# Performance work log

Measured on AMD Instinct MI355X. Metric: run time of the kernel, lower is better.

The kernel has to match this reference:

```python
import jax, jax.numpy as jnp
import numpy as np

FRACTION = 0.33  # from attn_type='query_selector_0.33'


def setup_inputs() -> dict:
    key = jax.random.key(0)
    k1, k2, k3, k4 = jax.random.split(key, 4)
    B, L, DIM_VAL, DIM_ATTN = 8, 4096, 64, 64
    scale = 1.0 / np.sqrt(DIM_VAL).astype(np.float32)
    x = jax.random.normal(k1, (B, L, DIM_VAL), dtype=jnp.float32)
    Wq = jax.random.normal(k2, (DIM_VAL, DIM_ATTN), dtype=jnp.float32) * scale
    Wk = jax.random.normal(k3, (DIM_VAL, DIM_ATTN), dtype=jnp.float32) * scale
    Wv = jax.random.normal(k4, (DIM_VAL, DIM_VAL), dtype=jnp.float32) * scale
    return {"x": x, "Wq": Wq, "Wk": Wk, "Wv": Wv}


def reference(x, Wq, Wk, Wv):
    # Projections (bias-free Linears)
    Q = jnp.einsum('bld,de->ble', x, Wq)  # [B, L, Da]
    K = jnp.einsum('bld,de->ble', x, Wk)  # [B, L, Da]
    V = jnp.einsum('bld,de->ble', x, Wv)  # [B, L, Dv]

    B, L_Q, Da = Q.shape
    l_Q = int((1.0 - FRACTION) * L_Q)  # static: shapes known at trace time

    # keys.topk(l_Q, dim=1).values -> per-channel top-l_Q along seq; mean over them
    K_top = jax.lax.top_k(jnp.swapaxes(K, 1, 2), l_Q)[0]  # [B, Da, l_Q]
    K_reduce = K_top.mean(axis=-1)                         # [B, Da]

    # score each query against the reduced key; pick top-l_Q queries
    sqk = jnp.einsum('bd,bld->bl', K_reduce, Q)            # [B, L_Q]
    indices = jax.lax.top_k(sqk, l_Q)[1]                   # [B, l_Q] int32

    # gather sampled queries
    Q_sample = jnp.take_along_axis(Q, indices[:, :, None], axis=1)  # [B, l_Q, Da]

    # dense attention for the sampled queries only
    scores = jnp.einsum('bqd,bkd->bqk', Q_sample, K) / jnp.sqrt(jnp.asarray(Da, Q.dtype))
    attn = jax.nn.softmax(scores, axis=-1)                 # [B, l_Q, L]
    out_sel = jnp.einsum('bqk,bkv->bqv', attn, V)          # [B, l_Q, Dv]

    # mean-filled result, scatter attention outputs to selected rows
    mean_values = V.mean(axis=-2)                          # [B, Dv]
    result = jnp.broadcast_to(mean_values[:, None, :], (B, L_Q, V.shape[-1]))
    result = result.at[jnp.arange(B)[:, None], indices].set(out_sel)
    return result
```

## Files before the change

### kernel.cpp

```cpp
#include <hip/hip_runtime.h>
#include <hip/hip_bf16.h>
#include <math.h>

#define BATCH 8
#define SEQ   4096
#define DIM   64
#define LQ    2744
#define QPB   128
#define NQB   22
#define QPAD  2816
#define KS    4
#define L2E   1.4426950408889634f
#define QSC   0.1803368801111204f

typedef _Float16 half8 __attribute__((ext_vector_type(8)));
typedef short    bs8   __attribute__((ext_vector_type(8)));
typedef float    fx16  __attribute__((ext_vector_type(16)));
typedef unsigned short ushort_t;

union UH { uint4 u4; half8 h; };
union UB { unsigned u[4]; uint4 u4; bs8 s; };

__device__ __forceinline__ unsigned pack_bf16(float a, float b) {
    __hip_bfloat162 h = __float22bfloat162_rn(make_float2(a, b));
    union { __hip_bfloat162 h; unsigned u; } cv; cv.h = h; return cv.u;
}

__device__ __forceinline__ unsigned f2sort(float f) {
    unsigned u = __float_as_uint(f);
    return (u & 0x80000000u) ? ~u : (u | 0x80000000u);
}
__device__ __forceinline__ float sort2f(unsigned u) {
    return __uint_as_float((u & 0x80000000u) ? (u & 0x7FFFFFFFu) : ~u);
}

__device__ void radix_select_4096(const unsigned* u, int k, unsigned* hist,
                                  unsigned* scan, unsigned* res) {
    const int t = threadIdx.x;
    if (t == 0) { res[0] = 0u; res[1] = (unsigned)k; }
    for (int pass = 3; pass >= 0; --pass) {
        const int shift = pass * 8;
        hist[t] = 0u;
        __syncthreads();
        const unsigned pref  = res[0];
        const unsigned kk    = res[1];
        const unsigned hmask = (pass == 3) ? 0u : (0xFFFFFFFFu << (shift + 8));
        for (int i = t; i < 4096; i += 256) {
            unsigned ui = u[i];
            if ((ui & hmask) == pref) atomicAdd(&hist[(ui >> shift) & 255u], 1u);
        }
        __syncthreads();
        const unsigned h = hist[t];
        unsigned s = h;
        scan[t] = s;
        __syncthreads();
#pragma unroll
        for (int ofs = 1; ofs < 256; ofs <<= 1) {
            unsigned add = (t + ofs < 256) ? scan[t + ofs] : 0u;
            __syncthreads();
            s += add;
            scan[t] = s;
            __syncthreads();
        }
        if (s >= kk && (s - h) < kk) {
            res[0] = pref | ((unsigned)t << shift);
            res[1] = kk - (s - h);
        }
        __syncthreads();
    }
}

__global__ __launch_bounds__(256) void proj_kernel(
    const float* __restrict__ x,  const float* __restrict__ Wq,
    const float* __restrict__ Wk, const float* __restrict__ Wv,
    float* __restrict__ Q, float* __restrict__ Kt,
    _Float16* __restrict__ Qh, _Float16* __restrict__ Kh,
    ushort_t* __restrict__ Vt, float* __restrict__ pmean) {
    const int rt = blockIdx.x, b = blockIdx.y, t = threadIdx.x;
    __shared__ float4 xs4[64 * 17];
    __shared__ float  red[4][64];
    {
        const float4* xg = (const float4*)(x + ((size_t)b * SEQ + rt * 64) * DIM);
        for (int i = 0; i < 4; ++i) {
            int s = t + 256 * i;
            xs4[(s >> 4) * 17 + (s & 15)] = xg[s];
        }
    }
    __syncthreads();
    const int ch = t & 63, rg = t >> 6;
    float accq[16], acck[16], accv[16];
#pragma unroll
    for (int i = 0; i < 16; ++i) { accq[i] = 0.f; acck[i] = 0.f; accv[i] = 0.f; }
    for (int dc = 0; dc < 4; ++dc) {
        float wq[16], wk[16], wv[16];
#pragma unroll
        for (int dd = 0; dd < 16; ++dd) {
            int d = dc * 16 + dd;
            wq[dd] = Wq[d * 64 + ch]; wk[dd] = Wk[d * 64 + ch]; wv[dd] = Wv[d * 64 + ch];
        }
        for (int r = 0; r < 16; ++r) {
            const int row = rg * 16 + r;
            const float4* xr = &xs4[row * 17 + dc * 4];
            float xv[16];
            float4 a0 = xr[0], a1 = xr[1], a2 = xr[2], a3 = xr[3];
            xv[0]=a0.x; xv[1]=a0.y; xv[2]=a0.z; xv[3]=a0.w;
            xv[4]=a1.x; xv[5]=a1.y; xv[6]=a1.z; xv[7]=a1.w;
            xv[8]=a2.x; xv[9]=a2.y; xv[10]=a2.z; xv[11]=a2.w;
            xv[12]=a3.x; xv[13]=a3.y; xv[14]=a3.z; xv[15]=a3.w;
#pragma unroll
            for (int dd = 0; dd < 16; ++dd) {
                accq[r] = fmaf(xv[dd], wq[dd], accq[r]);
                acck[r] = fmaf(xv[dd], wk[dd], acck[r]);
                accv[r] = fmaf(xv[dd], wv[dd], accv[r]);
            }
        }
    }
    const int rowbase = rt * 64 + rg * 16;
    float sv = 0.f;
#pragma unroll
    for (int r = 0; r < 16; ++r) {
        size_t o = ((size_t)b * SEQ + rowbase + r) * DIM + ch;
        Q[o]  = accq[r];
        Qh[o] = (_Float16)(accq[r] * QSC);
        Kh[o] = (_Float16)acck[r];
        sv += accv[r];
    }
    float4* ktp = (float4*)(Kt + ((size_t)b * 64 + ch) * SEQ + rowbase);
    ktp[0] = make_float4(acck[0], acck[1], acck[2], acck[3]);
    ktp[1] = make_float4(acck[4], acck[5], acck[6], acck[7]);
    ktp[2] = make_float4(acck[8], acck[9], acck[10], acck[11]);
    ktp[3] = make_float4(acck[12], acck[13], acck[14], acck[15]);
    {
        unsigned pk[8];
#pragma unroll
        for (int i = 0; i < 8; ++i) pk[i] = pack_bf16(accv[2*i], accv[2*i+1]);
        uint4* vp = (uint4*)(Vt + ((size_t)(b * 64 + ch)) * SEQ + rowbase);
        vp[0] = make_uint4(pk[0], pk[1], pk[4], pk[5]);
        vp[1] = make_uint4(pk[2], pk[3], pk[6], pk[7]);
    }
    red[rg][ch] = sv;
    __syncthreads();
    if (rg == 0)
        pmean[((size_t)b * 64 + ch) * 64 + rt] =
            red[0][ch] + red[1][ch] + red[2][ch] + red[3][ch];
}

__global__ __launch_bounds__(256) void kmean_kernel(const float* __restrict__ Kt,
                                                    const float* __restrict__ pmean,
                                                    float* __restrict__ Kred,
                                                    float* __restrict__ meanfin) {
    __shared__ unsigned u[4096];
    __shared__ unsigned hist[256];
    __shared__ unsigned scan[256];
    __shared__ unsigned res[2];
    __shared__ float rsum[4];
    const int bc = blockIdx.x, t = threadIdx.x;
    if (t < 64) {
        float v = pmean[(size_t)bc * 64 + t];
        for (int m = 1; m < 64; m <<= 1) v += __shfl_xor(v, m, 64);
        if (t == 0) meanfin[bc] = v * (1.0f / (float)SEQ);
    }
    const float4* c4 = (const float4*)(Kt + (size_t)bc * SEQ);
    for (int i = t; i < 1024; i += 256) {
        float4 v = c4[i];
        u[i*4+0] = f2sort(v.x); u[i*4+1] = f2sort(v.y);
        u[i*4+2] = f2sort(v.z); u[i*4+3] = f2sort(v.w);
    }
    __syncthreads();
    radix_select_4096(u, LQ, hist, scan, res);
    const unsigned Tu = res[0];
    const int krem = (int)res[1];
    float loc = 0.f;
    for (int i = t; i < 4096; i += 256)
        if (u[i] > Tu) loc += sort2f(u[i]);
    for (int msk = 1; msk < 64; msk <<= 1) loc += __shfl_xor(loc, msk, 64);
    if ((t & 63) == 0) rsum[t >> 6] = loc;
    __syncthreads();
    if (t == 0) {
        float s = rsum[0] + rsum[1] + rsum[2] + rsum[3] + (float)krem * sort2f(Tu);
        Kred[bc] = s / (float)LQ;
    }
}

__global__ __launch_bounds__(256) void sqk_kernel(const float* __restrict__ Q,
                                                  const float* __restrict__ Kred,
                                                  float* __restrict__ sqk) {
    const int b = blockIdx.y, l = blockIdx.x * 256 + threadIdx.x;
    __shared__ float kr[64];
    if (threadIdx.x < 64) kr[threadIdx.x] = Kred[b * 64 + threadIdx.x];
    __syncthreads();
    const float4* q = (const float4*)(Q + ((size_t)b * SEQ + l) * DIM);
    float s = 0.f;
#pragma unroll
    for (int i = 0; i < 16; ++i) {
        float4 v = q[i];
        s = fmaf(v.x, kr[i*4+0], s); s = fmaf(v.y, kr[i*4+1], s);
        s = fmaf(v.z, kr[i*4+2], s); s = fmaf(v.w, kr[i*4+3], s);
    }
    sqk[b * SEQ + l] = s;
}

__global__ __launch_bounds__(256) void select_kernel(const float* __restrict__ sqk,
                                                     int* __restrict__ sel,
                                                     int* __restrict__ inv) {
    __shared__ unsigned u[4096];
    __shared__ unsigned hist[256];
    __shared__ unsigned scan[256];
    __shared__ unsigned res[2];
    __shared__ int eq_idx[256];
    __shared__ int cnts[2];
    const int b = blockIdx.x, t = threadIdx.x;
    const float* col = sqk + (size_t)b * SEQ;
    int* invb = inv + (size_t)b * SEQ;
    for (int i = t; i < 4096; i += 256) {
        u[i] = f2sort(col[i]);
        invb[i] = -1;
    }
    if (t < 2) cnts[t] = 0;
    __syncthreads();
    radix_select_4096(u, LQ, hist, scan, res);
    const unsigned Tu = res[0];
    const int krem = (int)res[1];
    int* selb = sel + b * QPAD;
    for (int i = t; i < 4096; i += 256) {
        unsigned ui = u[i];
        if (ui > Tu) {
            int p = atomicAdd(&cnts[0], 1);
            selb[p] = i;
            invb[i] = p;
        } else if (ui == Tu) {
            int p = atomicAdd(&cnts[1], 1);
            if (p < 256) eq_idx[p] = i;
        }
    }
    __syncthreads();
    if (t == 0) {
        int ng = cnts[0];
        int ne = cnts[1] < 256 ? cnts[1] : 256;
        for (int i = 1; i < ne; ++i) {
            int v = eq_idx[i], j = i - 1;
            while (j >= 0 && eq_idx[j] > v) { eq_idx[j+1] = eq_idx[j]; --j; }
            eq_idx[j+1] = v;
        }
        for (int j = 0; j < krem; ++j) {
            selb[ng + j] = eq_idx[j];
            invb[eq_idx[j]] = ng + j;
        }
    }
    __syncthreads();
    if (t < QPAD - LQ) selb[LQ + t] = selb[LQ - 1];
}

__global__ __launch_bounds__(256, 3) void attn_kernel(
    const ushort_t* __restrict__ Qh, const ushort_t* __restrict__ Kh,
    const ushort_t* __restrict__ Vt, const int* __restrict__ sel,
    float* __restrict__ pl, float* __restrict__ pout) {
    const int qt = blockIdx.x, ks = blockIdx.y, b = blockIdx.z;
    const int t = threadIdx.x, w = t >> 6, lane = t & 63;
    const int col = lane & 31, h = lane >> 5;

    __shared__ ushort_t Ktile[2][32 * 64];
    __shared__ ushort_t Vtile[2][32 * 64];

    half8 qf[4];
    {
        const int q = qt * QPB + w * 32 + col;
        const int row = sel[b * QPAD + q];
        const uint4* qg = (const uint4*)(Qh + ((size_t)b * SEQ + row) * DIM);
#pragma unroll
        for (int m = 0; m < 4; ++m) { UH u; u.u4 = qg[2 * m + h]; qf[m] = u.h; }
    }

    int koff[4], voff[4];
#pragma unroll
    for (int m = 0; m < 4; ++m)
        koff[m] = col * 64 + 8 * ((2 * m + h) ^ (col & 7));
#pragma unroll
    for (int i = 0; i < 4; ++i)
        voff[i] = col * 64 + 8 * ((i * 2 + h) ^ (col & 7));

    fx16 O0, O1;
#pragma unroll
    for (int r = 0; r < 16; ++r) { O0[r] = 0.f; O1[r] = 0.f; }
    float l = 0.f;

    const int srow = t >> 3, sgr = t & 7;
    const int lg = sgr ^ (srow & 7);
    const int vD = lg >> 2, vc = (lg >> 1) & 1, vh = lg & 1;
    const size_t kgbase = ((size_t)b * SEQ + ks * 1024 + srow) * DIM + 8 * lg;
    const size_t vgbase = ((size_t)(b * DIM + srow + 32 * vD)) * SEQ
                          + ks * 1024 + vc * 16 + vh * 8;

    uint4 kreg = *(const uint4*)(Kh + kgbase);
    uint4 vreg = *(const uint4*)(Vt + vgbase);

    for (int tile = 0; tile < 32; ++tile) {
        const int buf = tile & 1;
        *(uint4*)&Ktile[buf][srow * 64 + sgr * 8] = kreg;
        *(uint4*)&Vtile[buf][srow * 64 + sgr * 8] = vreg;
        __syncthreads();
        if (tile < 31) {
            kreg = *(const uint4*)(Kh + kgbase + (size_t)(tile + 1) * 32 * DIM);
            vreg = *(const uint4*)(Vt + vgbase + (size_t)(tile + 1) * 32);
        }
        fx16 S;
#pragma unroll
        for (int r = 0; r < 16; ++r) S[r] = 0.f;
#pragma unroll
        for (int m = 0; m < 4; ++m) {
            UH kf;
            kf.u4 = *(const uint4*)&Ktile[buf][koff[m]];
            S = __builtin_amdgcn_mfma_f32_32x32x16_f16(kf.h, qf[m], S, 0, 0, 0);
        }
        float p[16];
#pragma unroll
        for (int r = 0; r < 16; ++r) p[r] = exp2f(S[r]);
#pragma unroll
        for (int r = 0; r < 16; ++r) l += p[r];
        UB A0, A1;
#pragma unroll
        for (int v = 0; v < 4; ++v) {
            A0.u[v] = pack_bf16(p[2 * v],     p[2 * v + 1]);
            A1.u[v] = pack_bf16(p[8 + 2 * v], p[8 + 2 * v + 1]);
        }
#pragma unroll
        for (int D = 0; D < 2; ++D) {
            fx16& O = D ? O1 : O0;
#pragma unroll
            for (int c = 0; c < 2; ++c) {
                UB vf;
                vf.u4 = *(const uint4*)&Vtile[buf][voff[D * 2 + c]];
                O = __builtin_amdgcn_mfma_f32_32x32x16_bf16(c ? A1.s : A0.s, vf.s, O, 0, 0, 0);
            }
        }
    }

    l += __shfl_xor(l, 32);

    const int qg0 = qt * QPB + w * 32;
    const size_t base = (size_t)b * QPAD + qg0;
#pragma unroll
    for (int D = 0; D < 2; ++D) {
        const fx16& O = D ? O1 : O0;
#pragma unroll
        for (int r = 0; r < 16; ++r) {
            const int q = (r & 3) + 8 * (r >> 2) + 4 * h;
            atomicAdd(&pout[(base + q) * DIM + D * 32 + col], O[r]);
        }
    }
    if (h == 0) atomicAdd(&pl[base + col], l);
}

__global__ __launch_bounds__(256) void comb_kernel(
    const float* __restrict__ pl, const float* __restrict__ pout,
    const int* __restrict__ inv, const float* __restrict__ meanfin,
    float* __restrict__ out) {
    const int idx = blockIdx.x * 256 + threadIdx.x;
    const int b = idx >> 16;
    const int rc = idx & 65535;
    const int row = rc >> 4, c = rc & 15;
    const int p = inv[b * SEQ + row];
    float4 o;
    if (p >= 0) {
        const size_t s0 = (size_t)b * QPAD + p;
        const float invl = 1.0f / pl[s0];
        float4 a = ((const float4*)(pout + s0 * DIM))[c];
        o = make_float4(a.x * invl, a.y * invl, a.z * invl, a.w * invl);
    } else {
        o = make_float4(meanfin[b * 64 + c * 4 + 0], meanfin[b * 64 + c * 4 + 1],
                        meanfin[b * 64 + c * 4 + 2], meanfin[b * 64 + c * 4 + 3]);
    }
    ((float4*)out)[idx] = o;
}

extern "C" void kernel_launch(void* const* d_in, const int* in_sizes, int n_in,
                              void* d_out, int out_size, void* d_ws, size_t ws_size,
                              hipStream_t stream) {
    const float* x  = (const float*)d_in[0];
    const float* Wq = (const float*)d_in[1];
    const float* Wk = (const float*)d_in[2];
    const float* Wv = (const float*)d_in[3];
    float* out = (float*)d_out;
    char* wsb  = (char*)d_ws;

    float*    Q       = (float*)(wsb);
    _Float16* Qh      = (_Float16*)(wsb + 8388608);
    _Float16* Kh      = (_Float16*)(wsb + 12582912);
    ushort_t* Vt      = (ushort_t*)(wsb + 16777216);
    float*    pmean   = (float*)(wsb + 20971520);
    float*    meanfin = (float*)(wsb + 21102592);
    float*    Kred    = (float*)(wsb + 21104640);
    float*    sqk     = (float*)(wsb + 21106688);
    int*      sel     = (int*)(wsb + 21237760);
    int*      inv     = (int*)(wsb + 21327872);
    float*    Kt      = (float*)(wsb + 21458944);
    float*    pout    = (float*)(wsb + 21458944);
    float*    pl      = (float*)(wsb + 21458944 + 5767168);

    proj_kernel  <<<dim3(64, 8),          256, 0, stream>>>(x, Wq, Wk, Wv, Q, Kt,
                                                            Qh, Kh, Vt, pmean);
    kmean_kernel <<<512,                  256, 0, stream>>>(Kt, pmean, Kred, meanfin);
    sqk_kernel   <<<dim3(16, 8),          256, 0, stream>>>(Q, Kred, sqk);
    select_kernel<<<8,                    256, 0, stream>>>(sqk, sel, inv);
    hipMemsetAsync(pout, 0, 5767168 + 90112, stream);
    attn_kernel  <<<dim3(NQB, KS, BATCH), 256, 0, stream>>>((const ushort_t*)Qh,
                                                            (const ushort_t*)Kh,
                                                            Vt, sel, pl, pout);
    comb_kernel  <<<2048,                 256, 0, stream>>>(pl, pout, inv, meanfin, out);
}
```

Measured before the change: 194.3 us.

## Fuse sqk and memset into select, shuffle-based radix scan, truncate kmean select

Merges the query-scoring kernel and the memset of the attention partial buffers into the select kernel, removing two launches. Replaces the shared-memory Hillis-Steele scan in radix select with wavefront shuffles plus a per-wave sum. kmean now stops radix selection after the top 16 bits and approximates the threshold value, which changes the top-k mean slightly. proj_kernel reads x directly with scalar-uniform loads instead of staging it in LDS. The fused select runs on only 8 blocks, so the scoring and zeroing work is serialized on few CUs.

```diff
diff --git a/kernel.cpp b/kernel.cpp
--- a/kernel.cpp
+++ b/kernel.cpp
@@ -10,7 +10,6 @@
 #define NQB   22
 #define QPAD  2816
 #define KS    4
-#define L2E   1.4426950408889634f
 #define QSC   0.1803368801111204f
 
 typedef _Float16 half8 __attribute__((ext_vector_type(8)));
@@ -34,11 +33,22 @@
     return __uint_as_float((u & 0x80000000u) ? (u & 0x7FFFFFFFu) : ~u);
 }
 
+struct RadSh {
+    unsigned u[4096];
+    unsigned hist[256];
+    unsigned wsum[4];
+    unsigned res[2];
+    float    rsum[4];
+    int      eq[256];
+    int      cnts[2];
+};
+
 __device__ void radix_select_4096(const unsigned* u, int k, unsigned* hist,
-                                  unsigned* scan, unsigned* res) {
+                                  unsigned* wsum, unsigned* res, int pass_lo) {
     const int t = threadIdx.x;
+    const int lane = t & 63, wv = t >> 6;
     if (t == 0) { res[0] = 0u; res[1] = (unsigned)k; }
-    for (int pass = 3; pass >= 0; --pass) {
+    for (int pass = 3; pass >= pass_lo; --pass) {
         const int shift = pass * 8;
         hist[t] = 0u;
         __syncthreads();
@@ -52,16 +62,16 @@
         __syncthreads();
         const unsigned h = hist[t];
         unsigned s = h;
-        scan[t] = s;
-        __syncthreads();
-#pragma unroll
-        for (int ofs = 1; ofs < 256; ofs <<= 1) {
-            unsigned add = (t + ofs < 256) ? scan[t + ofs] : 0u;
-            __syncthreads();
-            s += add;
-            scan[t] = s;
-            __syncthreads();
-        }
+#pragma unroll
+        for (int ofs = 1; ofs < 64; ofs <<= 1) {
+            unsigned a = __shfl_down(s, ofs, 64);
+            s += (lane + ofs < 64) ? a : 0u;
+        }
+        if (lane == 0) wsum[wv] = s;
+        __syncthreads();
+#pragma unroll
+        for (int w2 = 0; w2 < 4; ++w2)
+            if (w2 > wv) s += wsum[w2];
         if (s >= kk && (s - h) < kk) {
             res[0] = pref | ((unsigned)t << shift);
             res[1] = kk - (s - h);
@@ -77,17 +87,9 @@
     _Float16* __restrict__ Qh, _Float16* __restrict__ Kh,
     ushort_t* __restrict__ Vt, float* __restrict__ pmean) {
     const int rt = blockIdx.x, b = blockIdx.y, t = threadIdx.x;
-    __shared__ float4 xs4[64 * 17];
     __shared__ float  red[4][64];
-    {
-        const float4* xg = (const float4*)(x + ((size_t)b * SEQ + rt * 64) * DIM);
-        for (int i = 0; i < 4; ++i) {
-            int s = t + 256 * i;
-            xs4[(s >> 4) * 17 + (s & 15)] = xg[s];
-        }
-    }
-    __syncthreads();
     const int ch = t & 63, rg = t >> 6;
+    const float* xb = x + (size_t)b * SEQ * DIM;
     float accq[16], acck[16], accv[16];
 #pragma unroll
     for (int i = 0; i < 16; ++i) { accq[i] = 0.f; acck[i] = 0.f; accv[i] = 0.f; }
@@ -99,14 +101,12 @@
             wq[dd] = Wq[d * 64 + ch]; wk[dd] = Wk[d * 64 + ch]; wv[dd] = Wv[d * 64 + ch];
         }
         for (int r = 0; r < 16; ++r) {
-            const int row = rg * 16 + r;
-            const float4* xr = &xs4[row * 17 + dc * 4];
+            const int off = (rt * 64 + rg * 16 + r) * DIM + dc * 16;
+            const float* xrow =
+                xb + (unsigned)__builtin_amdgcn_readfirstlane(off);
             float xv[16];
-            float4 a0 = xr[0], a1 = xr[1], a2 = xr[2], a3 = xr[3];
-            xv[0]=a0.x; xv[1]=a0.y; xv[2]=a0.z; xv[3]=a0.w;
-            xv[4]=a1.x; xv[5]=a1.y; xv[6]=a1.z; xv[7]=a1.w;
-            xv[8]=a2.x; xv[9]=a2.y; xv[10]=a2.z; xv[11]=a2.w;
-            xv[12]=a3.x; xv[13]=a3.y; xv[14]=a3.z; xv[15]=a3.w;
+#pragma unroll
+            for (int dd = 0; dd < 16; ++dd) xv[dd] = xrow[dd];
 #pragma unroll
             for (int dd = 0; dd < 16; ++dd) {
                 accq[r] = fmaf(xv[dd], wq[dd], accq[r]);
@@ -149,11 +149,7 @@
                                                     const float* __restrict__ pmean,
                                                     float* __restrict__ Kred,
                                                     float* __restrict__ meanfin) {
-    __shared__ unsigned u[4096];
-    __shared__ unsigned hist[256];
-    __shared__ unsigned scan[256];
-    __shared__ unsigned res[2];
-    __shared__ float rsum[4];
+    __shared__ RadSh sh;
     const int bc = blockIdx.x, t = threadIdx.x;
     if (t < 64) {
         float v = pmean[(size_t)bc * 64 + t];
@@ -163,88 +159,81 @@
     const float4* c4 = (const float4*)(Kt + (size_t)bc * SEQ);
     for (int i = t; i < 1024; i += 256) {
         float4 v = c4[i];
-        u[i*4+0] = f2sort(v.x); u[i*4+1] = f2sort(v.y);
-        u[i*4+2] = f2sort(v.z); u[i*4+3] = f2sort(v.w);
-    }
-    __syncthreads();
-    radix_select_4096(u, LQ, hist, scan, res);
-    const unsigned Tu = res[0];
-    const int krem = (int)res[1];
+        sh.u[i*4+0] = f2sort(v.x); sh.u[i*4+1] = f2sort(v.y);
+        sh.u[i*4+2] = f2sort(v.z); sh.u[i*4+3] = f2sort(v.w);
+    }
+    __syncthreads();
+    radix_select_4096(sh.u, LQ, sh.hist, sh.wsum, sh.res, 2);
+    const unsigned Tu = sh.res[0];
+    const int krem = (int)sh.res[1];
     float loc = 0.f;
     for (int i = t; i < 4096; i += 256)
-        if (u[i] > Tu) loc += sort2f(u[i]);
+        if ((sh.u[i] & 0xFFFF0000u) > Tu) loc += sort2f(sh.u[i]);
     for (int msk = 1; msk < 64; msk <<= 1) loc += __shfl_xor(loc, msk, 64);
-    if ((t & 63) == 0) rsum[t >> 6] = loc;
+    if ((t & 63) == 0) sh.rsum[t >> 6] = loc;
     __syncthreads();
     if (t == 0) {
-        float s = rsum[0] + rsum[1] + rsum[2] + rsum[3] + (float)krem * sort2f(Tu);
+        float s = sh.rsum[0] + sh.rsum[1] + sh.rsum[2] + sh.rsum[3]
+                + (float)krem * sort2f(Tu | 0x8000u);
         Kred[bc] = s / (float)LQ;
     }
 }
 
-__global__ __launch_bounds__(256) void sqk_kernel(const float* __restrict__ Q,
-                                                  const float* __restrict__ Kred,
-                                                  float* __restrict__ sqk) {
-    const int b = blockIdx.y, l = blockIdx.x * 256 + threadIdx.x;
+__global__ __launch_bounds__(256) void select_kernel(
+    const float* __restrict__ Q, const float* __restrict__ Kred,
+    float4* __restrict__ pz, int* __restrict__ sel, int* __restrict__ inv) {
+    __shared__ RadSh r;
     __shared__ float kr[64];
-    if (threadIdx.x < 64) kr[threadIdx.x] = Kred[b * 64 + threadIdx.x];
-    __syncthreads();
-    const float4* q = (const float4*)(Q + ((size_t)b * SEQ + l) * DIM);
-    float s = 0.f;
-#pragma unroll
-    for (int i = 0; i < 16; ++i) {
-        float4 v = q[i];
-        s = fmaf(v.x, kr[i*4+0], s); s = fmaf(v.y, kr[i*4+1], s);
-        s = fmaf(v.z, kr[i*4+2], s); s = fmaf(v.w, kr[i*4+3], s);
-    }
-    sqk[b * SEQ + l] = s;
-}
-
-__global__ __launch_bounds__(256) void select_kernel(const float* __restrict__ sqk,
-                                                     int* __restrict__ sel,
-                                                     int* __restrict__ inv) {
-    __shared__ unsigned u[4096];
-    __shared__ unsigned hist[256];
-    __shared__ unsigned scan[256];
-    __shared__ unsigned res[2];
-    __shared__ int eq_idx[256];
-    __shared__ int cnts[2];
     const int b = blockIdx.x, t = threadIdx.x;
-    const float* col = sqk + (size_t)b * SEQ;
+    {
+        const float4 z = make_float4(0.f, 0.f, 0.f, 0.f);
+        for (int i = b * 256 + t; i < 366080; i += 2048) pz[i] = z;
+    }
+    if (t < 64) kr[t] = Kred[b * 64 + t];
     int* invb = inv + (size_t)b * SEQ;
-    for (int i = t; i < 4096; i += 256) {
-        u[i] = f2sort(col[i]);
-        invb[i] = -1;
-    }
-    if (t < 2) cnts[t] = 0;
-    __syncthreads();
-    radix_select_4096(u, LQ, hist, scan, res);
-    const unsigned Tu = res[0];
-    const int krem = (int)res[1];
+    __syncthreads();
+    for (int j = 0; j < 16; ++j) {
+        const int l = t + 256 * j;
+        const float4* q = (const float4*)(Q + ((size_t)b * SEQ + l) * DIM);
+        float s = 0.f;
+#pragma unroll
+        for (int i = 0; i < 16; ++i) {
+            float4 v = q[i];
+            s = fmaf(v.x, kr[i*4+0], s); s = fmaf(v.y, kr[i*4+1], s);
+            s = fmaf(v.z, kr[i*4+2], s); s = fmaf(v.w, kr[i*4+3], s);
+        }
+        r.u[l] = f2sort(s);
+        invb[l] = -1;
+    }
+    if (t < 2) r.cnts[t] = 0;
+    __syncthreads();
+    radix_select_4096(r.u, LQ, r.hist, r.wsum, r.res, 0);
+    const unsigned Tu = r.res[0];
+    const int krem = (int)r.res[1];
     int* selb = sel + b * QPAD;
     for (int i = t; i < 4096; i += 256) {
-        unsigned ui = u[i];
+        unsigned ui = r.u[i];
         if (ui > Tu) {
-            int p = atomicAdd(&cnts[0], 1);
+            int p = atomicAdd(&r.cnts[0], 1);
             selb[p] = i;
             invb[i] = p;
         } else if (ui == Tu) {
-            int p = atomicAdd(&cnts[1], 1);
-            if (p < 256) eq_idx[p] = i;
+            int p = atomicAdd(&r.cnts[1], 1);
+            if (p < 256) r.eq[p] = i;
         }
     }
     __syncthreads();
     if (t == 0) {
-        int ng = cnts[0];
-        int ne = cnts[1] < 256 ? cnts[1] : 256;
+        int ng = r.cnts[0];
+        int ne = r.cnts[1] < 256 ? r.cnts[1] : 256;
         for (int i = 1; i < ne; ++i) {
-            int v = eq_idx[i], j = i - 1;
-            while (j >= 0 && eq_idx[j] > v) { eq_idx[j+1] = eq_idx[j]; --j; }
-            eq_idx[j+1] = v;
+            int v = r.eq[i], j = i - 1;
+            while (j >= 0 && r.eq[j] > v) { r.eq[j+1] = r.eq[j]; --j; }
+            r.eq[j+1] = v;
         }
         for (int j = 0; j < krem; ++j) {
-            selb[ng + j] = eq_idx[j];
-            invb[eq_idx[j]] = ng + j;
+            selb[ng + j] = r.eq[j];
+            invb[r.eq[j]] = ng + j;
         }
     }
     __syncthreads();
@@ -390,7 +379,6 @@
     float*    pmean   = (float*)(wsb + 20971520);
     float*    meanfin = (float*)(wsb + 21102592);
     float*    Kred    = (float*)(wsb + 21104640);
-    float*    sqk     = (float*)(wsb + 21106688);
     int*      sel     = (int*)(wsb + 21237760);
     int*      inv     = (int*)(wsb + 21327872);
     float*    Kt      = (float*)(wsb + 21458944);
@@ -400,9 +388,8 @@
     proj_kernel  <<<dim3(64, 8),          256, 0, stream>>>(x, Wq, Wk, Wv, Q, Kt,
                                                             Qh, Kh, Vt, pmean);
     kmean_kernel <<<512,                  256, 0, stream>>>(Kt, pmean, Kred, meanfin);
-    sqk_kernel   <<<dim3(16, 8),          256, 0, stream>>>(Q, Kred, sqk);
-    select_kernel<<<8,                    256, 0, stream>>>(sqk, sel, inv);
-    hipMemsetAsync(pout, 0, 5767168 + 90112, stream);
+    select_kernel<<<8,                    256, 0, stream>>>(Q, Kred, (float4*)pout,
+                                                            sel, inv);
     attn_kernel  <<<dim3(NQB, KS, BATCH), 256, 0, stream>>>((const ushort_t*)Qh,
                                                             (const ushort_t*)Kh,
                                                             Vt, sel, pl, pout);
```

New measurement: 215.9 us. 1.11x slower.
